# Performance work log

Measured on AMD Instinct MI355X. Metric: run time of the kernel, lower is better.

The kernel has to match this reference:

```python
import jax, jax.numpy as jnp
import numpy as np

B, S, E, H = 2, 2048, 1024, 16
D = E // H  # head dim = 64


def setup_inputs() -> dict:
    key = jax.random.key(0)
    ks = jax.random.split(key, 9)
    sc = 0.02
    return {
        "inputs": jax.random.normal(ks[0], (B, S, E), jnp.float32),
        "Wq": jax.random.normal(ks[1], (E, E), jnp.float32) * sc,
        "bq": jnp.zeros((E,), jnp.float32),
        "Wk": jax.random.normal(ks[2], (E, E), jnp.float32) * sc,
        "bk": jnp.zeros((E,), jnp.float32),
        "Wv": jax.random.normal(ks[3], (E, E), jnp.float32) * sc,
        "bv": jnp.zeros((E,), jnp.float32),
        "Wo": jax.random.normal(ks[4], (E, E), jnp.float32) * sc,
        "bo": jnp.zeros((E,), jnp.float32),
    }


def _split_heads(x):
    # [B, S, E] -> [B, H, S, D]
    b, s, _ = x.shape
    return x.reshape(b, s, H, D).transpose(0, 2, 1, 3)


def reference(inputs, Wq, bq, Wk, bk, Wv, bv, Wo, bo):
    q = _split_heads(inputs @ Wq + bq)
    k = _split_heads(inputs @ Wk + bk)
    v = _split_heads(inputs @ Wv + bv)

    # scaled dot-product scores: [B, H, S, S]
    score = jnp.einsum("bhqd,bhkd->bhqk", q, k) / jnp.sqrt(jnp.float32(D))

    # causal mask, exactly as the original: score*mask - 10000*(1-mask)
    i = jnp.arange(S)[:, None]
    j = jnp.arange(S)[None, :]
    mask = (i >= j).astype(score.dtype)  # square case of i >= j - S + S
    score = score * mask - 10000.0 * (1.0 - mask)

    weights = jax.nn.softmax(score, axis=-1)
    attn = jnp.einsum("bhqk,bhkd->bhqd", weights, v)  # [B, H, S, D]
    attn = attn.transpose(0, 2, 1, 3).reshape(inputs.shape[0], S, E)
    return attn @ Wo + bo
```

## Files before the change

kernel.cpp:

```cpp
#include <hip/hip_runtime.h>
#include <stdint.h>

#define Bc 2
#define Sc 2048
#define Ec 1024
#define Hc 16
#define Dc 64
#define Mc (Bc*Sc)

typedef __attribute__((ext_vector_type(4))) float f32x4;
typedef __attribute__((ext_vector_type(8))) short bf16x8v;

#define SCL 0.1803368801f

__device__ __forceinline__ unsigned short f2bf(float f){
  unsigned int u = __float_as_uint(f);
  u += 0x7FFFu + ((u >> 16) & 1u);
  return (unsigned short)(u >> 16);
}

__global__ __launch_bounds__(256) void k_cvt(const float* __restrict__ x,
                                             unsigned short* __restrict__ y, int n4){
  int i = blockIdx.x * 256 + threadIdx.x;
  if (i >= n4) return;
  float4 v = ((const float4*)x)[i];
  ushort4 o;
  o.x = f2bf(v.x); o.y = f2bf(v.y); o.z = f2bf(v.z); o.w = f2bf(v.w);
  ((ushort4*)y)[i] = o;
}

__global__ __launch_bounds__(256) void k_wt(const float* __restrict__ W0, const float* __restrict__ W1,
                                            const float* __restrict__ W2, const float* __restrict__ W3,
                                            unsigned short* __restrict__ out){
  __shared__ float st[64][65];
  const float* W = (blockIdx.z==0)?W0 : (blockIdx.z==1)?W1 : (blockIdx.z==2)?W2 : W3;
  unsigned short* o = out + (size_t)blockIdx.z * Ec * Ec;
  int k0 = blockIdx.y*64, n0 = blockIdx.x*64;
  int t = threadIdx.x;
  #pragma unroll
  for (int i=0;i<16;i++){ int lin=i*256+t; int r=lin>>6, c=lin&63;
    st[r][c] = W[(size_t)(k0+r)*Ec + n0+c]; }
  __syncthreads();
  #pragma unroll
  for (int i=0;i<16;i++){ int lin=i*256+t; int nn=lin>>6, kk=lin&63;
    o[(size_t)(n0+nn)*Ec + k0+kk] = f2bf(st[kk][nn]); }
}

template<int MODE, int BN>
__global__ __launch_bounds__(256) void k_gemm(const unsigned short* __restrict__ A,
                                              const unsigned short* __restrict__ WTbase,
                                              const float* __restrict__ b0,
                                              const float* __restrict__ b1,
                                              const float* __restrict__ b2,
                                              void* __restrict__ outv){
  constexpr int NSN = BN/32;
  __shared__ unsigned short sA[2][128*32];
  __shared__ unsigned short sB[2][BN*32];
  int z = blockIdx.z;
  const unsigned short* WT = WTbase + (size_t)z * Ec * Ec;
  const float* bias = (z==0)?b0 : (z==1)?b1 : b2;
  int bm = blockIdx.y, bn = blockIdx.x;
  int t = threadIdx.x, w = t>>6, lane = t&63, quad = lane>>4, m16 = lane&15;
  int wm = w>>1, wn = w&1;
  f32x4 acc[4][NSN];
  #pragma unroll
  for (int i=0;i<4;i++)
    #pragma unroll
    for (int j=0;j<NSN;j++) acc[i][j] = (f32x4){0.f,0.f,0.f,0.f};

  auto stage = [&](int kt, int buf){
    #pragma unroll
    for (int i=0;i<2;i++){
      int cb = (w*2 + i)*64;
      int L = cb + lane;
      int row = L>>2, c = (L&3)*8;
      const unsigned short* ga = A + (size_t)(bm*128 + row)*Ec + kt*32 + c;
      __builtin_amdgcn_global_load_lds((const __attribute__((address_space(1))) void*)ga,
          (__attribute__((address_space(3))) void*)(&sA[buf][0] + cb*8), 16, 0, 0);
    }
    #pragma unroll
    for (int i=0;i<BN/64;i++){
      int cb = (w*(BN/64) + i)*64;
      int L = cb + lane;
      int row = L>>2, c = (L&3)*8;
      const unsigned short* gb = WT + (size_t)(bn*BN + row)*Ec + kt*32 + c;
      __builtin_amdgcn_global_load_lds((const __attribute__((address_space(1))) void*)gb,
          (__attribute__((address_space(3))) void*)(&sB[buf][0] + cb*8), 16, 0, 0);
    }
  };

  stage(0, 0);
  for (int kt=0; kt<Ec/32; ++kt){
    int cur = kt & 1;
    __syncthreads();
    if (kt+1 < Ec/32) stage(kt+1, cur^1);
    bf16x8v af[4], bfr[NSN];
    #pragma unroll
    for (int s=0;s<4;s++)
      af[s]  = *(const bf16x8v*)(&sA[cur][0] + (wm*64 + s*16 + m16)*32 + quad*8);
    #pragma unroll
    for (int s=0;s<NSN;s++)
      bfr[s] = *(const bf16x8v*)(&sB[cur][0] + (wn*(BN/2) + s*16 + m16)*32 + quad*8);
    #pragma unroll
    for (int sm=0;sm<4;sm++)
      #pragma unroll
      for (int sn=0;sn<NSN;sn++)
        acc[sm][sn] = __builtin_amdgcn_mfma_f32_16x16x32_bf16(af[sm], bfr[sn], acc[sm][sn], 0,0,0);
  }
  #pragma unroll
  for (int sm=0;sm<4;sm++){
    int row0 = bm*128 + wm*64 + sm*16 + quad*4;
    #pragma unroll
    for (int sn=0;sn<NSN;sn++){
      int col = bn*BN + wn*(BN/2) + sn*16 + m16;
      float bb = bias[col];
      if (MODE==0){
        unsigned short* Out = (unsigned short*)outv + (size_t)z * (size_t)Mc * Ec;
        int bidx = row0 >> 11;
        int h = col >> 6, d = col & 63;
        if (z == 2){
          int s0 = row0 & (Sc-1);
          ushort4 pk;
          pk.x = f2bf(acc[sm][sn][0] + bb);
          pk.y = f2bf(acc[sm][sn][1] + bb);
          pk.z = f2bf(acc[sm][sn][2] + bb);
          pk.w = f2bf(acc[sm][sn][3] + bb);
          *(ushort4*)(Out + (((size_t)bidx*Hc + h)*Dc + d)*Sc + s0) = pk;
        } else {
          float sc_ = (z==0) ? SCL : 1.0f;
          #pragma unroll
          for (int r=0;r<4;r++){
            int s = (row0 + r) & (Sc-1);
            Out[(((size_t)bidx*Hc + h)*Sc + s)*Dc + d] = f2bf((acc[sm][sn][r] + bb)*sc_);
          }
        }
      } else {
        float* Out = (float*)outv;
        #pragma unroll
        for (int r=0;r<4;r++)
          Out[(size_t)(row0+r)*Ec + col] = acc[sm][sn][r] + bb;
      }
    }
  }
}

__device__ __forceinline__ void attn_tile(const unsigned short* sK, const unsigned short* sVT,
                                          unsigned short* pw, bf16x8v qf0, bf16x8v qf1,
                                          bf16x8v ones, f32x4& li, f32x4* Oa,
                                          int kbase, int qw, int quad, int m16){
  int sw = m16 & 7;
  f32x4 sc[4];
  #pragma unroll
  for (int sm=0;sm<4;sm++){
    int row = sm*16 + m16;
    bf16x8v kf0 = *(const bf16x8v*)(sK + row*64 + ((quad  )^sw)*8);
    bf16x8v kf1 = *(const bf16x8v*)(sK + row*64 + ((quad+4)^sw)*8);
    f32x4 a = (f32x4){0.f,0.f,0.f,0.f};
    a = __builtin_amdgcn_mfma_f32_16x16x32_bf16(kf0, qf0, a, 0,0,0);
    a = __builtin_amdgcn_mfma_f32_16x16x32_bf16(kf1, qf1, a, 0,0,0);
    sc[sm] = a;
  }
  if (kbase + 63 > qw){
    #pragma unroll
    for (int sm=0;sm<4;sm++)
      #pragma unroll
      for (int r=0;r<4;r++){
        int kg = kbase + sm*16 + quad*4 + r;
        float p = exp2f(sc[sm][r]);
        sc[sm][r] = (kg <= qw + m16) ? p : 0.0f;
      }
  } else {
    #pragma unroll
    for (int sm=0;sm<4;sm++)
      #pragma unroll
      for (int r=0;r<4;r++) sc[sm][r] = exp2f(sc[sm][r]);
  }

  #pragma unroll
  for (int sm=0;sm<4;sm++){
    ushort4 pk;
    pk.x = f2bf(sc[sm][0]); pk.y = f2bf(sc[sm][1]);
    pk.z = f2bf(sc[sm][2]); pk.w = f2bf(sc[sm][3]);
    int chunk = sm*2 + (quad>>1);
    *(ushort4*)(pw + m16*64 + (chunk^sw)*8 + (quad&1)*4) = pk;
  }
  bf16x8v pf0 = *(const bf16x8v*)(pw + m16*64 + ((quad  )^sw)*8);
  bf16x8v pf1 = *(const bf16x8v*)(pw + m16*64 + ((quad+4)^sw)*8);

  li = __builtin_amdgcn_mfma_f32_16x16x32_bf16(pf0, ones, li, 0,0,0);
  li = __builtin_amdgcn_mfma_f32_16x16x32_bf16(pf1, ones, li, 0,0,0);

  #pragma unroll
  for (int tt=0;tt<4;tt++){
    int rowv = tt*16 + m16;
    bf16x8v vf0 = *(const bf16x8v*)(sVT + rowv*64 + ((quad  )^sw)*8);
    bf16x8v vf1 = *(const bf16x8v*)(sVT + rowv*64 + ((quad+4)^sw)*8);
    Oa[tt] = __builtin_amdgcn_mfma_f32_16x16x32_bf16(pf0, vf0, Oa[tt], 0,0,0);
    Oa[tt] = __builtin_amdgcn_mfma_f32_16x16x32_bf16(pf1, vf1, Oa[tt], 0,0,0);
  }
}

__global__ __launch_bounds__(256,2) void k_attn(const unsigned short* __restrict__ Qb,
                                                const unsigned short* __restrict__ Kb,
                                                const unsigned short* __restrict__ VTb,
                                                unsigned short* __restrict__ Ob){
  __shared__ unsigned short sK [64*64];
  __shared__ unsigned short sVT[64*64];
  __shared__ unsigned short sP [4][16*64];
  int bh = blockIdx.y;
  int qtA = (int)blockIdx.x;
  int qtB = 31 - qtA;
  size_t base = (size_t)bh * Sc * Dc;
  const unsigned short* Q  = Qb  + base;
  const unsigned short* K  = Kb  + base;
  const unsigned short* VT = VTb + base;
  int t = threadIdx.x, w = t>>6, lane = t&63, quad = lane>>4, m16 = lane&15;
  int qwA = qtA*64 + w*16;
  int qwB = qtB*64 + w*16;

  bf16x8v qA0 = *(const bf16x8v*)(Q + (size_t)(qwA + m16)*Dc + quad*8);
  bf16x8v qA1 = *(const bf16x8v*)(Q + (size_t)(qwA + m16)*Dc + 32 + quad*8);
  bf16x8v qB0 = *(const bf16x8v*)(Q + (size_t)(qwB + m16)*Dc + quad*8);
  bf16x8v qB1 = *(const bf16x8v*)(Q + (size_t)(qwB + m16)*Dc + 32 + quad*8);

  bf16x8v ones;
  #pragma unroll
  for (int i=0;i<8;i++) ones[i] = (short)0x3F80;

  f32x4 OaA[4], OaB[4];
  #pragma unroll
  for (int i=0;i<4;i++){ OaA[i] = (f32x4){0.f,0.f,0.f,0.f}; OaB[i] = (f32x4){0.f,0.f,0.f,0.f}; }
  f32x4 liA = (f32x4){0.f,0.f,0.f,0.f}, liB = (f32x4){0.f,0.f,0.f,0.f};

  unsigned short* pw = &sP[w][0];

  for (int kt=0; kt<=qtB; ++kt){
    int kbase = kt*64;
    #pragma unroll
    for (int i=0;i<2;i++){
      int cb = (w*2 + i)*64;
      int L = cb + lane;
      int row = L>>3, p = L&7, c = p ^ (row&7);
      const unsigned short* gk = K  + (size_t)(kbase+row)*Dc + c*8;
      const unsigned short* gv = VT + (size_t)row*Sc + kbase + c*8;
      __builtin_amdgcn_global_load_lds((const __attribute__((address_space(1))) void*)gk,
          (__attribute__((address_space(3))) void*)(sK + cb*8), 16, 0, 0);
      __builtin_amdgcn_global_load_lds((const __attribute__((address_space(1))) void*)gv,
          (__attribute__((address_space(3))) void*)(sVT + cb*8), 16, 0, 0);
    }
    __syncthreads();

    if (kt <= qtA)
      attn_tile(sK, sVT, pw, qA0, qA1, ones, liA, OaA, kbase, qwA, quad, m16);
    attn_tile(sK, sVT, pw, qB0, qB1, ones, liB, OaB, kbase, qwB, quad, m16);

    __syncthreads();
  }

  int b = bh >> 4, h = bh & 15;
  float iA[4], iB[4];
  #pragma unroll
  for (int r=0;r<4;r++){ iA[r] = 1.0f/liA[r]; iB[r] = 1.0f/liB[r]; }
  #pragma unroll
  for (int tt=0;tt<4;tt++)
    #pragma unroll
    for (int r=0;r<4;r++){
      int e = h*64 + tt*16 + m16;
      int sA_ = qwA + quad*4 + r;
      int sB_ = qwB + quad*4 + r;
      Ob[((size_t)b*Sc + sA_)*Ec + e] = f2bf(OaA[tt][r]*iA[r]);
      Ob[((size_t)b*Sc + sB_)*Ec + e] = f2bf(OaB[tt][r]*iB[r]);
    }
}

extern "C" void kernel_launch(void* const* d_in, const int* in_sizes, int n_in,
                              void* d_out, int out_size, void* d_ws, size_t ws_size,
                              hipStream_t stream){
  const float* X  = (const float*)d_in[0];
  const float* Wq = (const float*)d_in[1];
  const float* bq = (const float*)d_in[2];
  const float* Wk = (const float*)d_in[3];
  const float* bk = (const float*)d_in[4];
  const float* Wv = (const float*)d_in[5];
  const float* bv = (const float*)d_in[6];
  const float* Wo = (const float*)d_in[7];
  const float* bo = (const float*)d_in[8];

  uint8_t* ws = (uint8_t*)d_ws;
  unsigned short* Xb  = (unsigned short*)(ws);
  unsigned short* WT4 = (unsigned short*)(ws + (size_t)(8u<<20));
  unsigned short* QKV = (unsigned short*)(ws + (size_t)(16u<<20));
  unsigned short* ATT = (unsigned short*)(ws + (size_t)(40u<<20));

  k_cvt<<<dim3((Mc*Ec/4)/256), 256, 0, stream>>>(X, Xb, Mc*Ec/4);
  k_wt<<<dim3(16,16,4), 256, 0, stream>>>(Wq, Wk, Wv, Wo, WT4);
  k_gemm<0,128><<<dim3(8,32,3), 256, 0, stream>>>(Xb, WT4, bq, bk, bv, (void*)QKV);
  k_attn<<<dim3(16,32), 256, 0, stream>>>(QKV, QKV + (size_t)Mc*Ec, QKV + 2*(size_t)Mc*Ec, ATT);
  k_gemm<1,64><<<dim3(16,32,1), 256, 0, stream>>>(ATT, WT4 + (size_t)3*Ec*Ec, bo, bo, bo, d_out);
}
```

Before: 205.7 us.

## Fuse prep kernels and split paired attention query tiles into separate blocks

Merges the input bf16 conversion and weight-transpose kernels into one launch, removing one kernel launch. The attention kernel no longer pairs query tile i with tile 31-i in one block. Each block now handles a single query tile, with the longest tiles scheduled first, and the grid doubles to 1024 blocks with launch bounds raised to 4 waves per SIMD. This gives more parallelism and occupancy, but each K/V tile is now loaded from global memory once per query tile instead of being shared by two, and the work per block becomes uneven.

New measurement: 220.0 us. +7.0%, slower.

```diff
diff --git a/kernel.cpp b/kernel.cpp
--- a/kernel.cpp
+++ b/kernel.cpp
@@ -19,31 +19,33 @@
   return (unsigned short)(u >> 16);
 }
 
-__global__ __launch_bounds__(256) void k_cvt(const float* __restrict__ x,
-                                             unsigned short* __restrict__ y, int n4){
-  int i = blockIdx.x * 256 + threadIdx.x;
-  if (i >= n4) return;
-  float4 v = ((const float4*)x)[i];
-  ushort4 o;
-  o.x = f2bf(v.x); o.y = f2bf(v.y); o.z = f2bf(v.z); o.w = f2bf(v.w);
-  ((ushort4*)y)[i] = o;
-}
-
-__global__ __launch_bounds__(256) void k_wt(const float* __restrict__ W0, const float* __restrict__ W1,
-                                            const float* __restrict__ W2, const float* __restrict__ W3,
-                                            unsigned short* __restrict__ out){
+__global__ __launch_bounds__(256) void k_prep(const float* __restrict__ X,
+                                              unsigned short* __restrict__ Xb,
+                                              const float* __restrict__ W0, const float* __restrict__ W1,
+                                              const float* __restrict__ W2, const float* __restrict__ W3,
+                                              unsigned short* __restrict__ WT4){
   __shared__ float st[64][65];
-  const float* W = (blockIdx.z==0)?W0 : (blockIdx.z==1)?W1 : (blockIdx.z==2)?W2 : W3;
-  unsigned short* o = out + (size_t)blockIdx.z * Ec * Ec;
-  int k0 = blockIdx.y*64, n0 = blockIdx.x*64;
-  int t = threadIdx.x;
-  #pragma unroll
-  for (int i=0;i<16;i++){ int lin=i*256+t; int r=lin>>6, c=lin&63;
-    st[r][c] = W[(size_t)(k0+r)*Ec + n0+c]; }
-  __syncthreads();
-  #pragma unroll
-  for (int i=0;i<16;i++){ int lin=i*256+t; int nn=lin>>6, kk=lin&63;
-    o[(size_t)(n0+nn)*Ec + k0+kk] = f2bf(st[kk][nn]); }
+  int bx = blockIdx.x, t = threadIdx.x;
+  if (bx < 4096){
+    int i = bx*256 + t;
+    float4 v = ((const float4*)X)[i];
+    ushort4 o;
+    o.x = f2bf(v.x); o.y = f2bf(v.y); o.z = f2bf(v.z); o.w = f2bf(v.w);
+    ((ushort4*)Xb)[i] = o;
+  } else {
+    int id = bx - 4096;
+    int z = id >> 8, rem = id & 255;
+    int k0 = (rem >> 4)*64, n0 = (rem & 15)*64;
+    const float* W = (z==0)?W0 : (z==1)?W1 : (z==2)?W2 : W3;
+    unsigned short* o = WT4 + (size_t)z * Ec * Ec;
+    #pragma unroll
+    for (int i=0;i<16;i++){ int lin=i*256+t; int r=lin>>6, c=lin&63;
+      st[r][c] = W[(size_t)(k0+r)*Ec + n0+c]; }
+    __syncthreads();
+    #pragma unroll
+    for (int i=0;i<16;i++){ int lin=i*256+t; int nn=lin>>6, kk=lin&63;
+      o[(size_t)(n0+nn)*Ec + k0+kk] = f2bf(st[kk][nn]); }
+  }
 }
 
 template<int MODE, int BN>
@@ -200,7 +202,7 @@
   }
 }
 
-__global__ __launch_bounds__(256,2) void k_attn(const unsigned short* __restrict__ Qb,
+__global__ __launch_bounds__(256,4) void k_attn(const unsigned short* __restrict__ Qb,
                                                 const unsigned short* __restrict__ Kb,
                                                 const unsigned short* __restrict__ VTb,
                                                 unsigned short* __restrict__ Ob){
@@ -208,33 +210,29 @@
   __shared__ unsigned short sVT[64*64];
   __shared__ unsigned short sP [4][16*64];
   int bh = blockIdx.y;
-  int qtA = (int)blockIdx.x;
-  int qtB = 31 - qtA;
+  int qt = 31 - (int)blockIdx.x;
   size_t base = (size_t)bh * Sc * Dc;
   const unsigned short* Q  = Qb  + base;
   const unsigned short* K  = Kb  + base;
   const unsigned short* VT = VTb + base;
   int t = threadIdx.x, w = t>>6, lane = t&63, quad = lane>>4, m16 = lane&15;
-  int qwA = qtA*64 + w*16;
-  int qwB = qtB*64 + w*16;
-
-  bf16x8v qA0 = *(const bf16x8v*)(Q + (size_t)(qwA + m16)*Dc + quad*8);
-  bf16x8v qA1 = *(const bf16x8v*)(Q + (size_t)(qwA + m16)*Dc + 32 + quad*8);
-  bf16x8v qB0 = *(const bf16x8v*)(Q + (size_t)(qwB + m16)*Dc + quad*8);
-  bf16x8v qB1 = *(const bf16x8v*)(Q + (size_t)(qwB + m16)*Dc + 32 + quad*8);
+  int qw = qt*64 + w*16;
+
+  bf16x8v qf0 = *(const bf16x8v*)(Q + (size_t)(qw + m16)*Dc + quad*8);
+  bf16x8v qf1 = *(const bf16x8v*)(Q + (size_t)(qw + m16)*Dc + 32 + quad*8);
 
   bf16x8v ones;
   #pragma unroll
   for (int i=0;i<8;i++) ones[i] = (short)0x3F80;
 
-  f32x4 OaA[4], OaB[4];
-  #pragma unroll
-  for (int i=0;i<4;i++){ OaA[i] = (f32x4){0.f,0.f,0.f,0.f}; OaB[i] = (f32x4){0.f,0.f,0.f,0.f}; }
-  f32x4 liA = (f32x4){0.f,0.f,0.f,0.f}, liB = (f32x4){0.f,0.f,0.f,0.f};
+  f32x4 Oa[4];
+  #pragma unroll
+  for (int i=0;i<4;i++) Oa[i] = (f32x4){0.f,0.f,0.f,0.f};
+  f32x4 li = (f32x4){0.f,0.f,0.f,0.f};
 
   unsigned short* pw = &sP[w][0];
 
-  for (int kt=0; kt<=qtB; ++kt){
+  for (int kt=0; kt<=qt; ++kt){
     int kbase = kt*64;
     #pragma unroll
     for (int i=0;i<2;i++){
@@ -250,26 +248,22 @@
     }
     __syncthreads();
 
-    if (kt <= qtA)
-      attn_tile(sK, sVT, pw, qA0, qA1, ones, liA, OaA, kbase, qwA, quad, m16);
-    attn_tile(sK, sVT, pw, qB0, qB1, ones, liB, OaB, kbase, qwB, quad, m16);
+    attn_tile(sK, sVT, pw, qf0, qf1, ones, li, Oa, kbase, qw, quad, m16);
 
     __syncthreads();
   }
 
   int b = bh >> 4, h = bh & 15;
-  float iA[4], iB[4];
-  #pragma unroll
-  for (int r=0;r<4;r++){ iA[r] = 1.0f/liA[r]; iB[r] = 1.0f/liB[r]; }
+  float iv[4];
+  #pragma unroll
+  for (int r=0;r<4;r++) iv[r] = 1.0f/li[r];
   #pragma unroll
   for (int tt=0;tt<4;tt++)
     #pragma unroll
     for (int r=0;r<4;r++){
       int e = h*64 + tt*16 + m16;
-      int sA_ = qwA + quad*4 + r;
-      int sB_ = qwB + quad*4 + r;
-      Ob[((size_t)b*Sc + sA_)*Ec + e] = f2bf(OaA[tt][r]*iA[r]);
-      Ob[((size_t)b*Sc + sB_)*Ec + e] = f2bf(OaB[tt][r]*iB[r]);
+      int s = qw + quad*4 + r;
+      Ob[((size_t)b*Sc + s)*Ec + e] = f2bf(Oa[tt][r]*iv[r]);
     }
 }
 
@@ -292,9 +286,8 @@
   unsigned short* QKV = (unsigned short*)(ws + (size_t)(16u<<20));
   unsigned short* ATT = (unsigned short*)(ws + (size_t)(40u<<20));
 
-  k_cvt<<<dim3((Mc*Ec/4)/256), 256, 0, stream>>>(X, Xb, Mc*Ec/4);
-  k_wt<<<dim3(16,16,4), 256, 0, stream>>>(Wq, Wk, Wv, Wo, WT4);
+  k_prep<<<dim3(5120), 256, 0, stream>>>(X, Xb, Wq, Wk, Wv, Wo, WT4);
   k_gemm<0,128><<<dim3(8,32,3), 256, 0, stream>>>(Xb, WT4, bq, bk, bv, (void*)QKV);
-  k_attn<<<dim3(16,32), 256, 0, stream>>>(QKV, QKV + (size_t)Mc*Ec, QKV + 2*(size_t)Mc*Ec, ATT);
+  k_attn<<<dim3(32,32), 256, 0, stream>>>(QKV, QKV + (size_t)Mc*Ec, QKV + 2*(size_t)Mc*Ec, ATT);
   k_gemm<1,64><<<dim3(16,32,1), 256, 0, stream>>>(ATT, WT4 + (size_t)3*Ec*Ec, bo, bo, bo, d_out);
 }
```
